# Kernel tuning notes

Measured on AMD Instinct MI355X. Metric: run time of the kernel, lower is better.

Reference implementation:

```python
import jax, jax.numpy as jnp
import numpy as np

N_NODES = 100000
N_EDGES = 3200000
D_IN, D_HID, D_OUT = 128, 128, 128


def setup_inputs() -> dict:
    key = jax.random.key(0)
    ks = jax.random.split(key, 8)
    x = jax.random.normal(ks[0], (N_NODES, D_IN), dtype=jnp.float32)
    edge_index = jax.random.randint(ks[1], (2, N_EDGES), 0, N_NODES, dtype=jnp.int64)
    def lin(k, din, dout):
        # glorot-ish init for GCNConv weight
        s = 1.0 / np.sqrt(din)
        return jax.random.uniform(k, (din, dout), jnp.float32, -s, s)
    W0 = lin(ks[2], D_IN, D_HID)
    b0 = jnp.zeros((D_HID,), jnp.float32)
    W1 = lin(ks[3], D_HID, D_HID)
    b1 = jnp.zeros((D_HID,), jnp.float32)
    W2 = lin(ks[4], D_HID, D_OUT)
    b2 = jnp.zeros((D_OUT,), jnp.float32)
    return {"x": x, "edge_index": edge_index, "W0": W0, "b0": b0,
            "W1": W1, "b1": b1, "W2": W2, "b2": b2}


def _gcn_norm(edge_index, n_nodes):
    # PyG gcn_norm with self-loops: deg over target index, sym normalization
    loop = jnp.arange(n_nodes, dtype=edge_index.dtype)
    src = jnp.concatenate([edge_index[0], loop])
    dst = jnp.concatenate([edge_index[1], loop])
    deg = jax.ops.segment_sum(jnp.ones_like(dst, dtype=jnp.float32), dst,
                              num_segments=n_nodes)
    dinv = jnp.where(deg > 0, jax.lax.rsqrt(deg), 0.0)
    norm = dinv[src] * dinv[dst]  # [E + N]
    return src, dst, norm


def _gcn_conv(h, src, dst, norm, W, b, n_nodes):
    h = h @ W                                   # [N, dout] transform first
    msg = h[src] * norm[:, None]                # gather + scale
    out = jax.ops.segment_sum(msg, dst, num_segments=n_nodes)  # scatter-add
    return out + b


def reference(x, edge_index, W0, b0, W1, b1, W2, b2):
    n = x.shape[0]
    src, dst, norm = _gcn_norm(edge_index, n)
    # layer 0
    h = jax.nn.relu(_gcn_conv(x, src, dst, norm, W0, b0, n))
    # residual middle layer (dropout is identity in eval mode)
    h = jax.nn.relu(_gcn_conv(h, src, dst, norm, W1, b1, n) + h)
    # output layer
    return _gcn_conv(h, src, dst, norm, W2, b2, n)
```

## Files before the change

### kernel.cpp

```cpp
#include <hip/hip_runtime.h>
#include <hip/hip_fp16.h>

#define D 128
typedef unsigned long long ull;
typedef _Float16 half8 __attribute__((ext_vector_type(8)));
typedef _Float16 half4v __attribute__((ext_vector_type(4)));
typedef float f32x4 __attribute__((ext_vector_type(4)));

#define KPOS(k4) (((k4) & ~31) + ((((k4) & 15) >> 2) << 3) + ((((k4) >> 4) & 1) << 2))

__global__ void k_zero_int(int* p, int n) {
  int i = blockIdx.x * blockDim.x + threadIdx.x;
  if (i < n) p[i] = 0;
}

__global__ void k_deg_count8(const int* __restrict__ ei, int* __restrict__ deg8,
                             int E, int N) {
  const int c = blockIdx.x & 7;
  const int m = blockIdx.x >> 3;
  const int nb = gridDim.x >> 3;
  const int cE = (E + 7) >> 3;
  const int base = c * cE;
  int lim = E - base;
  if (lim > cE) lim = cE;
  int* dg = deg8 + (size_t)c * N;
  for (int i = m * 256 + threadIdx.x; i < lim; i += nb * 256) {
    int d = __builtin_nontemporal_load(&ei[E + base + i]);
    atomicAdd(&dg[d], 1);
  }
}

__global__ void k_deg_reduce(const int* __restrict__ deg8, int* __restrict__ deg, int N) {
  int i = blockIdx.x * blockDim.x + threadIdx.x;
  if (i >= N) return;
  int s = 0;
#pragma unroll
  for (int c = 0; c < 8; c++) s += deg8[(size_t)c * N + i];
  deg[i] = s;
}

__global__ void k_scan_part(const int* __restrict__ deg, int* __restrict__ part, int n) {
  __shared__ int sd[256];
  int base = blockIdx.x * 2048 + threadIdx.x * 8;
  int s = 0;
#pragma unroll
  for (int k = 0; k < 8; k++) {
    int idx = base + k;
    if (idx < n) s += deg[idx];
  }
  sd[threadIdx.x] = s;
  __syncthreads();
  for (int off = 128; off > 0; off >>= 1) {
    if (threadIdx.x < off) sd[threadIdx.x] += sd[threadIdx.x + off];
    __syncthreads();
  }
  if (threadIdx.x == 0) part[blockIdx.x] = sd[0];
}

__global__ void k_scan_offsets(int* __restrict__ part, int nparts,
                               int* __restrict__ rowptr, int n) {
  __shared__ int sd[256];
  int v = (threadIdx.x < nparts) ? part[threadIdx.x] : 0;
  sd[threadIdx.x] = v;
  __syncthreads();
  for (int off = 1; off < 256; off <<= 1) {
    int t = (threadIdx.x >= off) ? sd[threadIdx.x - off] : 0;
    __syncthreads();
    sd[threadIdx.x] += t;
    __syncthreads();
  }
  if (threadIdx.x < nparts) part[threadIdx.x] = sd[threadIdx.x] - v;
  if (threadIdx.x == 0) rowptr[n] = sd[255];
}

__global__ void k_scan_final(const int* __restrict__ deg, const int* __restrict__ part,
                             int* __restrict__ rowptr, int n) {
  __shared__ int sd[256];
  int base = blockIdx.x * 2048 + threadIdx.x * 8;
  int loc[8];
  int s = 0;
#pragma unroll
  for (int k = 0; k < 8; k++) {
    int idx = base + k;
    loc[k] = (idx < n) ? deg[idx] : 0;
    s += loc[k];
  }
  sd[threadIdx.x] = s;
  __syncthreads();
  for (int off = 1; off < 256; off <<= 1) {
    int t = (threadIdx.x >= off) ? sd[threadIdx.x - off] : 0;
    __syncthreads();
    sd[threadIdx.x] += t;
    __syncthreads();
  }
  int run = part[blockIdx.x] + sd[threadIdx.x] - s;
#pragma unroll
  for (int k = 0; k < 8; k++) {
    int idx = base + k;
    if (idx < n) {
      rowptr[idx] = run;
      run += loc[k];
    }
  }
}

__global__ void k_dinv(const int* __restrict__ rowptr, float* __restrict__ dinv, int n) {
  int i = blockIdx.x * blockDim.x + threadIdx.x;
  if (i < n) dinv[i] = rsqrtf((float)(rowptr[i + 1] - rowptr[i]) + 1.0f);
}

__global__ void k_cursor8_init(const int* __restrict__ rowptr, const int* __restrict__ deg8,
                               int* __restrict__ cursor8, int N) {
  int v = blockIdx.x * blockDim.x + threadIdx.x;
  if (v >= N) return;
  int run = rowptr[v];
#pragma unroll
  for (int c = 0; c < 8; c++) {
    cursor8[(size_t)c * N + v] = run;
    run += deg8[(size_t)c * N + v];
  }
}

__global__ void k_csr_fill_1p(const int* __restrict__ ei, int* __restrict__ cursor8,
                              int* __restrict__ csr, int E, int N) {
  const int c = blockIdx.x & 7;
  const int m = blockIdx.x >> 3;
  const int nb = gridDim.x >> 3;
  const int cE = (E + 7) >> 3;
  const int base = c * cE;
  int lim = E - base;
  if (lim > cE) lim = cE;
  int* cur = cursor8 + (size_t)c * N;
  for (int i = m * 256 + threadIdx.x; i < lim; i += nb * 256) {
    int d = __builtin_nontemporal_load(&ei[E + base + i]);
    int s = __builtin_nontemporal_load(&ei[base + i]);
    int pos = atomicAdd(&cur[d], 1);
    csr[pos] = s;
  }
}

template <int HALF_IN>
__launch_bounds__(256, 2)
__global__ void k_gemm_mfma(const void* __restrict__ Av, const float* __restrict__ W,
                            const float* __restrict__ dinv, __half* __restrict__ Th, int n) {
  __shared__ _Float16 Al[128 * 136];
  __shared__ _Float16 Bl[128 * 136];
  const int tid = threadIdx.x;
  const int row0 = blockIdx.x * 128;

  if (HALF_IN) {
    const _Float16* A = (const _Float16*)Av;
    for (int i = tid; i < 2048; i += 256) {
      int r = i >> 4;
      int k8 = (i & 15) << 3;
      half8 v = {0, 0, 0, 0, 0, 0, 0, 0};
      if (row0 + r < n) v = *(const half8*)&A[(size_t)(row0 + r) * D + k8];
      *(half4v*)&Al[r * 136 + KPOS(k8)]     = (half4v){v[0], v[1], v[2], v[3]};
      *(half4v*)&Al[r * 136 + KPOS(k8 + 4)] = (half4v){v[4], v[5], v[6], v[7]};
    }
  } else {
    const float* A = (const float*)Av;
    for (int i = tid; i < 4096; i += 256) {
      int r = i >> 5;
      int k4 = (i & 31) << 2;
      float4 v = make_float4(0.f, 0.f, 0.f, 0.f);
      if (row0 + r < n) v = ((const float4*)A)[(size_t)(row0 + r) * 32 + (i & 31)];
      *(half4v*)&Al[r * 136 + KPOS(k4)] =
          (half4v){(_Float16)v.x, (_Float16)v.y, (_Float16)v.z, (_Float16)v.w};
    }
  }
  for (int i = tid; i < 4096; i += 256) {
    int c = i & 127;
    int k4 = (i >> 7) << 2;
    float w0 = W[(k4 + 0) * D + c];
    float w1 = W[(k4 + 1) * D + c];
    float w2 = W[(k4 + 2) * D + c];
    float w3 = W[(k4 + 3) * D + c];
    *(half4v*)&Bl[c * 136 + KPOS(k4)] =
        (half4v){(_Float16)w0, (_Float16)w1, (_Float16)w2, (_Float16)w3};
  }
  __syncthreads();

  const int w = tid >> 6;
  const int lane = tid & 63;
  const int g = lane >> 4;
  const int q = lane & 15;

  f32x4 acc[2][8];
#pragma unroll
  for (int mt = 0; mt < 2; mt++)
#pragma unroll
    for (int nt = 0; nt < 8; nt++) acc[mt][nt] = (f32x4){0.f, 0.f, 0.f, 0.f};

#pragma unroll
  for (int kt = 0; kt < 4; kt++) {
    half8 a[2], b[8];
#pragma unroll
    for (int mt = 0; mt < 2; mt++)
      a[mt] = *(const half8*)&Al[(w * 32 + mt * 16 + q) * 136 + kt * 32 + g * 8];
#pragma unroll
    for (int nt = 0; nt < 8; nt++)
      b[nt] = *(const half8*)&Bl[(nt * 16 + q) * 136 + kt * 32 + g * 8];
#pragma unroll
    for (int mt = 0; mt < 2; mt++)
#pragma unroll
      for (int nt = 0; nt < 8; nt++)
        acc[mt][nt] = __builtin_amdgcn_mfma_f32_16x16x32_f16(a[mt], b[nt], acc[mt][nt], 0, 0, 0);
  }

#pragma unroll
  for (int mt = 0; mt < 2; mt++) {
    int baseRow = row0 + w * 32 + mt * 16 + g * 4;
    float dv[4];
#pragma unroll
    for (int r = 0; r < 4; r++) dv[r] = (baseRow + r < n) ? dinv[baseRow + r] : 0.f;
#pragma unroll
    for (int nt = 0; nt < 8; nt++) {
      int col = nt * 16 + q;
#pragma unroll
      for (int r = 0; r < 4; r++) {
        int gr = baseRow + r;
        if (gr < n) Th[(size_t)gr * D + col] = (__half)(acc[mt][nt][r] * dv[r]);
      }
    }
  }
}

template <int MODE>
__launch_bounds__(256)
__global__ void k_aggregate(const int* __restrict__ rowptr, const int* __restrict__ csr,
                            const float* __restrict__ dinv, const __half* __restrict__ th,
                            const float* __restrict__ b, const __half* __restrict__ resh,
                            __half* __restrict__ outh, float* __restrict__ outf, int n) {
  int node = blockIdx.x * 16 + (threadIdx.x >> 4);
  if (node >= n) return;
  const int l16 = threadIdx.x & 15;

  int beg = rowptr[node];
  int end = rowptr[node + 1];
  float dd = dinv[node];

  const float4* t4 = (const float4*)th;

  float a0, a1, a2, a3, a4, a5, a6, a7;
  {
    float4 raw = t4[(size_t)node * 16 + l16];
    const __half2* hp = (const __half2*)&raw;
    float2 f0 = __half22float2(hp[0]);
    float2 f1 = __half22float2(hp[1]);
    float2 f2 = __half22float2(hp[2]);
    float2 f3 = __half22float2(hp[3]);
    a0 = f0.x; a1 = f0.y; a2 = f1.x; a3 = f1.y;
    a4 = f2.x; a5 = f2.y; a6 = f3.x; a7 = f3.y;
  }

#define ACC_ROW(raw)                                  \
  {                                                   \
    const __half2* hp = (const __half2*)&(raw);       \
    float2 f0 = __half22float2(hp[0]);                \
    float2 f1 = __half22float2(hp[1]);                \
    float2 f2 = __half22float2(hp[2]);                \
    float2 f3 = __half22float2(hp[3]);                \
    a0 += f0.x; a1 += f0.y; a2 += f1.x; a3 += f1.y;   \
    a4 += f2.x; a5 += f2.y; a6 += f3.x; a7 += f3.y;   \
  }

  int j = beg;
  for (; j + 8 <= end; j += 8) {
    float4 r0, r1, r2, r3, r4, r5, r6, r7;
    {
      int s0 = __builtin_nontemporal_load(&csr[j + 0]);
      int s1 = __builtin_nontemporal_load(&csr[j + 1]);
      int s2 = __builtin_nontemporal_load(&csr[j + 2]);
      int s3 = __builtin_nontemporal_load(&csr[j + 3]);
      int s4 = __builtin_nontemporal_load(&csr[j + 4]);
      int s5 = __builtin_nontemporal_load(&csr[j + 5]);
      int s6 = __builtin_nontemporal_load(&csr[j + 6]);
      int s7 = __builtin_nontemporal_load(&csr[j + 7]);
      r0 = t4[(size_t)(unsigned)s0 * 16 + l16];
      r1 = t4[(size_t)(unsigned)s1 * 16 + l16];
      r2 = t4[(size_t)(unsigned)s2 * 16 + l16];
      r3 = t4[(size_t)(unsigned)s3 * 16 + l16];
      r4 = t4[(size_t)(unsigned)s4 * 16 + l16];
      r5 = t4[(size_t)(unsigned)s5 * 16 + l16];
      r6 = t4[(size_t)(unsigned)s6 * 16 + l16];
      r7 = t4[(size_t)(unsigned)s7 * 16 + l16];
    }
    ACC_ROW(r0) ACC_ROW(r1) ACC_ROW(r2) ACC_ROW(r3)
    ACC_ROW(r4) ACC_ROW(r5) ACC_ROW(r6) ACC_ROW(r7)
  }
  for (; j + 4 <= end; j += 4) {
    int s0 = __builtin_nontemporal_load(&csr[j + 0]);
    int s1 = __builtin_nontemporal_load(&csr[j + 1]);
    int s2 = __builtin_nontemporal_load(&csr[j + 2]);
    int s3 = __builtin_nontemporal_load(&csr[j + 3]);
    float4 r0 = t4[(size_t)(unsigned)s0 * 16 + l16];
    float4 r1 = t4[(size_t)(unsigned)s1 * 16 + l16];
    float4 r2 = t4[(size_t)(unsigned)s2 * 16 + l16];
    float4 r3 = t4[(size_t)(unsigned)s3 * 16 + l16];
    ACC_ROW(r0) ACC_ROW(r1) ACC_ROW(r2) ACC_ROW(r3)
  }
  for (; j < end; ++j) {
    int s = __builtin_nontemporal_load(&csr[j]);
    float4 r = t4[(size_t)(unsigned)s * 16 + l16];
    ACC_ROW(r)
  }
#undef ACC_ROW

  const float4* b4 = (const float4*)b;
  float4 bb0 = b4[l16 * 2];
  float4 bb1 = b4[l16 * 2 + 1];
  float o0 = fmaf(a0, dd, bb0.x), o1 = fmaf(a1, dd, bb0.y);
  float o2 = fmaf(a2, dd, bb0.z), o3 = fmaf(a3, dd, bb0.w);
  float o4 = fmaf(a4, dd, bb1.x), o5 = fmaf(a5, dd, bb1.y);
  float o6 = fmaf(a6, dd, bb1.z), o7 = fmaf(a7, dd, bb1.w);

  if (MODE == 1) {
    float4 raw = ((const float4*)resh)[(size_t)node * 16 + l16];
    const __half2* hp = (const __half2*)&raw;
    float2 f0 = __half22float2(hp[0]);
    float2 f1 = __half22float2(hp[1]);
    float2 f2 = __half22float2(hp[2]);
    float2 f3 = __half22float2(hp[3]);
    o0 += f0.x; o1 += f0.y; o2 += f1.x; o3 += f1.y;
    o4 += f2.x; o5 += f2.y; o6 += f3.x; o7 += f3.y;
  }
  if (MODE == 0 || MODE == 1) {
    o0 = fmaxf(o0, 0.f); o1 = fmaxf(o1, 0.f); o2 = fmaxf(o2, 0.f); o3 = fmaxf(o3, 0.f);
    o4 = fmaxf(o4, 0.f); o5 = fmaxf(o5, 0.f); o6 = fmaxf(o6, 0.f); o7 = fmaxf(o7, 0.f);
    union { __half2 h[4]; float4 f; } pk;
    pk.h[0] = __floats2half2_rn(o0, o1);
    pk.h[1] = __floats2half2_rn(o2, o3);
    pk.h[2] = __floats2half2_rn(o4, o5);
    pk.h[3] = __floats2half2_rn(o6, o7);
    ((float4*)outh)[(size_t)node * 16 + l16] = pk.f;
  } else {
    ((float4*)outf)[(size_t)node * 32 + l16 * 2] = make_float4(o0, o1, o2, o3);
    ((float4*)outf)[(size_t)node * 32 + l16 * 2 + 1] = make_float4(o4, o5, o6, o7);
  }
}

extern "C" void kernel_launch(void* const* d_in, const int* in_sizes, int n_in,
                              void* d_out, int out_size, void* d_ws, size_t ws_size,
                              hipStream_t stream) {
  const float* x  = (const float*)d_in[0];
  const int*   ei = (const int*)d_in[1];
  const float* W0 = (const float*)d_in[2];
  const float* b0 = (const float*)d_in[3];
  const float* W1 = (const float*)d_in[4];
  const float* b1 = (const float*)d_in[5];
  const float* W2 = (const float*)d_in[6];
  const float* b2 = (const float*)d_in[7];
  float* out = (float*)d_out;

  const int N = in_sizes[0] / D;
  const int E = in_sizes[1] / 2;

  char* wsb = (char*)d_ws;
  auto alloc = [&](size_t bytes) {
    char* p = wsb;
    wsb += ((bytes + 255) & ~(size_t)255);
    return p;
  };
  int*    rowptr  = (int*)alloc((N + 1) * 4);
  int*    deg     = (int*)alloc(N * 4);
  int*    part    = (int*)alloc(256 * 4);
  float*  dinv    = (float*)alloc(N * 4);
  int*    deg8    = (int*)alloc((size_t)8 * N * 4);
  int*    cursor8 = (int*)alloc((size_t)8 * N * 4);
  int*    csr     = (int*)alloc((size_t)E * 4);
  __half* th      = (__half*)alloc((size_t)N * D * 2);
  __half* g1h     = (__half*)alloc((size_t)N * D * 2);
  __half* g2h     = (__half*)alloc((size_t)N * D * 2);

  dim3 b256(256);
  int gN   = (N + 255) / 256;
  int gN8  = (8 * N + 255) / 256;
  int gGem = (N + 127) / 128;
  int gAgg = (N + 15) / 16;
  int nparts = (N + 2047) / 2048;

  k_zero_int<<<gN8, b256, 0, stream>>>(deg8, 8 * N);
  k_deg_count8<<<8 * 256, b256, 0, stream>>>(ei, deg8, E, N);
  k_deg_reduce<<<gN, b256, 0, stream>>>(deg8, deg, N);
  k_scan_part<<<nparts, b256, 0, stream>>>(deg, part, N);
  k_scan_offsets<<<1, b256, 0, stream>>>(part, nparts, rowptr, N);
  k_scan_final<<<nparts, b256, 0, stream>>>(deg, part, rowptr, N);
  k_dinv<<<gN, b256, 0, stream>>>(rowptr, dinv, N);
  k_cursor8_init<<<gN, b256, 0, stream>>>(rowptr, deg8, cursor8, N);
  k_csr_fill_1p<<<8 * 256, b256, 0, stream>>>(ei, cursor8, csr, E, N);

  k_gemm_mfma<0><<<gGem, b256, 0, stream>>>(x, W0, dinv, th, N);
  k_aggregate<0><<<gAgg, b256, 0, stream>>>(rowptr, csr, dinv, th, b0, nullptr, g1h, nullptr, N);

  k_gemm_mfma<1><<<gGem, b256, 0, stream>>>(g1h, W1, dinv, th, N);
  k_aggregate<1><<<gAgg, b256, 0, stream>>>(rowptr, csr, dinv, th, b1, g1h, g2h, nullptr, N);

  k_gemm_mfma<1><<<gGem, b256, 0, stream>>>(g2h, W2, dinv, th, N);
  k_aggregate<2><<<gAgg, b256, 0, stream>>>(rowptr, csr, dinv, th, b2, nullptr, nullptr, out, N);
}
```

Measured before the change: 819.1 us.

## Fill CSR per-chunk contiguously then reorder into per-node rows

Instead of scattering source indices straight into the final per-node CSR rows, each of the 8 edge chunks now writes into its own chunk-major region, whose offsets come from a global scan over the 8*N per-chunk degrees. A follow-up reorder kernel then copies each node's eight segments into the final CSR. The aim is for the scatter writes to land in more local regions and so cut cache-line contention during the fill. In exchange it adds an extra E-sized buffer, a second scan, a copy kernel and a reorder pass in which one thread serially copies each node's edges.

```diff
diff --git a/kernel.cpp b/kernel.cpp
--- a/kernel.cpp
+++ b/kernel.cpp
@@ -12,6 +12,11 @@
 __global__ void k_zero_int(int* p, int n) {
   int i = blockIdx.x * blockDim.x + threadIdx.x;
   if (i < n) p[i] = 0;
+}
+
+__global__ void k_copy_int(const int* __restrict__ a, int* __restrict__ b, int n) {
+  int i = blockIdx.x * blockDim.x + threadIdx.x;
+  if (i < n) b[i] = a[i];
 }
 
 __global__ void k_deg_count8(const int* __restrict__ ei, int* __restrict__ deg8,
@@ -39,14 +44,15 @@
   deg[i] = s;
 }
 
-__global__ void k_scan_part(const int* __restrict__ deg, int* __restrict__ part, int n) {
+template <int ITEMS>
+__global__ void k_scan_part(const int* __restrict__ v, int* __restrict__ part, int n) {
   __shared__ int sd[256];
-  int base = blockIdx.x * 2048 + threadIdx.x * 8;
+  int base = blockIdx.x * (256 * ITEMS) + threadIdx.x * ITEMS;
   int s = 0;
 #pragma unroll
-  for (int k = 0; k < 8; k++) {
+  for (int k = 0; k < ITEMS; k++) {
     int idx = base + k;
-    if (idx < n) s += deg[idx];
+    if (idx < n) s += v[idx];
   }
   sd[threadIdx.x] = s;
   __syncthreads();
@@ -58,7 +64,7 @@
 }
 
 __global__ void k_scan_offsets(int* __restrict__ part, int nparts,
-                               int* __restrict__ rowptr, int n) {
+                               int* __restrict__ outp, int n) {
   __shared__ int sd[256];
   int v = (threadIdx.x < nparts) ? part[threadIdx.x] : 0;
   sd[threadIdx.x] = v;
@@ -70,19 +76,20 @@
     __syncthreads();
   }
   if (threadIdx.x < nparts) part[threadIdx.x] = sd[threadIdx.x] - v;
-  if (threadIdx.x == 0) rowptr[n] = sd[255];
-}
-
-__global__ void k_scan_final(const int* __restrict__ deg, const int* __restrict__ part,
-                             int* __restrict__ rowptr, int n) {
+  if (threadIdx.x == 0) outp[n] = sd[255];
+}
+
+template <int ITEMS>
+__global__ void k_scan_final(const int* __restrict__ v, const int* __restrict__ part,
+                             int* __restrict__ outp, int n) {
   __shared__ int sd[256];
-  int base = blockIdx.x * 2048 + threadIdx.x * 8;
-  int loc[8];
+  int base = blockIdx.x * (256 * ITEMS) + threadIdx.x * ITEMS;
+  int loc[ITEMS];
   int s = 0;
 #pragma unroll
-  for (int k = 0; k < 8; k++) {
+  for (int k = 0; k < ITEMS; k++) {
     int idx = base + k;
-    loc[k] = (idx < n) ? deg[idx] : 0;
+    loc[k] = (idx < n) ? v[idx] : 0;
     s += loc[k];
   }
   sd[threadIdx.x] = s;
@@ -95,34 +102,22 @@
   }
   int run = part[blockIdx.x] + sd[threadIdx.x] - s;
 #pragma unroll
-  for (int k = 0; k < 8; k++) {
+  for (int k = 0; k < ITEMS; k++) {
     int idx = base + k;
     if (idx < n) {
-      rowptr[idx] = run;
+      outp[idx] = run;
       run += loc[k];
     }
   }
 }
 
-__global__ void k_dinv(const int* __restrict__ rowptr, float* __restrict__ dinv, int n) {
+__global__ void k_dinv(const int* __restrict__ deg, float* __restrict__ dinv, int n) {
   int i = blockIdx.x * blockDim.x + threadIdx.x;
-  if (i < n) dinv[i] = rsqrtf((float)(rowptr[i + 1] - rowptr[i]) + 1.0f);
-}
-
-__global__ void k_cursor8_init(const int* __restrict__ rowptr, const int* __restrict__ deg8,
-                               int* __restrict__ cursor8, int N) {
-  int v = blockIdx.x * blockDim.x + threadIdx.x;
-  if (v >= N) return;
-  int run = rowptr[v];
-#pragma unroll
-  for (int c = 0; c < 8; c++) {
-    cursor8[(size_t)c * N + v] = run;
-    run += deg8[(size_t)c * N + v];
-  }
-}
-
-__global__ void k_csr_fill_1p(const int* __restrict__ ei, int* __restrict__ cursor8,
-                              int* __restrict__ csr, int E, int N) {
+  if (i < n) dinv[i] = rsqrtf((float)deg[i] + 1.0f);
+}
+
+__global__ void k_fill8(const int* __restrict__ ei, int* __restrict__ cursor8,
+                        int* __restrict__ csr8, int E, int N) {
   const int c = blockIdx.x & 7;
   const int m = blockIdx.x >> 3;
   const int nb = gridDim.x >> 3;
@@ -135,7 +130,20 @@
     int d = __builtin_nontemporal_load(&ei[E + base + i]);
     int s = __builtin_nontemporal_load(&ei[base + i]);
     int pos = atomicAdd(&cur[d], 1);
-    csr[pos] = s;
+    csr8[pos] = s;
+  }
+}
+
+__global__ void k_reorder(const int* __restrict__ S, const int* __restrict__ rowptr,
+                          const int* __restrict__ csr8, int* __restrict__ csr, int N) {
+  int v = blockIdx.x * blockDim.x + threadIdx.x;
+  if (v >= N) return;
+  int dst = rowptr[v];
+#pragma unroll
+  for (int c = 0; c < 8; c++) {
+    int b = S[(size_t)c * N + v];
+    int e = S[(size_t)c * N + v + 1];
+    for (int j = b; j < e; j++) csr[dst++] = __builtin_nontemporal_load(&csr8[j]);
   }
 }
 
@@ -365,30 +373,38 @@
   int*    rowptr  = (int*)alloc((N + 1) * 4);
   int*    deg     = (int*)alloc(N * 4);
   int*    part    = (int*)alloc(256 * 4);
+  int*    part2   = (int*)alloc(256 * 4);
   float*  dinv    = (float*)alloc(N * 4);
   int*    deg8    = (int*)alloc((size_t)8 * N * 4);
+  int*    S       = (int*)alloc(((size_t)8 * N + 1) * 4);
   int*    cursor8 = (int*)alloc((size_t)8 * N * 4);
+  int*    csr8    = (int*)alloc((size_t)E * 4);
   int*    csr     = (int*)alloc((size_t)E * 4);
   __half* th      = (__half*)alloc((size_t)N * D * 2);
   __half* g1h     = (__half*)alloc((size_t)N * D * 2);
   __half* g2h     = (__half*)alloc((size_t)N * D * 2);
 
   dim3 b256(256);
-  int gN   = (N + 255) / 256;
-  int gN8  = (8 * N + 255) / 256;
-  int gGem = (N + 127) / 128;
-  int gAgg = (N + 15) / 16;
-  int nparts = (N + 2047) / 2048;
+  int gN    = (N + 255) / 256;
+  int gN8   = (8 * N + 255) / 256;
+  int gGem  = (N + 127) / 128;
+  int gAgg  = (N + 15) / 16;
+  int np1   = (N + 2047) / 2048;
+  int np16  = (8 * N + 4095) / 4096;
 
   k_zero_int<<<gN8, b256, 0, stream>>>(deg8, 8 * N);
   k_deg_count8<<<8 * 256, b256, 0, stream>>>(ei, deg8, E, N);
   k_deg_reduce<<<gN, b256, 0, stream>>>(deg8, deg, N);
-  k_scan_part<<<nparts, b256, 0, stream>>>(deg, part, N);
-  k_scan_offsets<<<1, b256, 0, stream>>>(part, nparts, rowptr, N);
-  k_scan_final<<<nparts, b256, 0, stream>>>(deg, part, rowptr, N);
-  k_dinv<<<gN, b256, 0, stream>>>(rowptr, dinv, N);
-  k_cursor8_init<<<gN, b256, 0, stream>>>(rowptr, deg8, cursor8, N);
-  k_csr_fill_1p<<<8 * 256, b256, 0, stream>>>(ei, cursor8, csr, E, N);
+  k_scan_part<8><<<np1, b256, 0, stream>>>(deg, part, N);
+  k_scan_offsets<<<1, b256, 0, stream>>>(part, np1, rowptr, N);
+  k_scan_final<8><<<np1, b256, 0, stream>>>(deg, part, rowptr, N);
+  k_scan_part<16><<<np16, b256, 0, stream>>>(deg8, part2, 8 * N);
+  k_scan_offsets<<<1, b256, 0, stream>>>(part2, np16, S, 8 * N);
+  k_scan_final<16><<<np16, b256, 0, stream>>>(deg8, part2, S, 8 * N);
+  k_dinv<<<gN, b256, 0, stream>>>(deg, dinv, N);
+  k_copy_int<<<gN8, b256, 0, stream>>>(S, cursor8, 8 * N);
+  k_fill8<<<8 * 256, b256, 0, stream>>>(ei, cursor8, csr8, E, N);
+  k_reorder<<<gN, b256, 0, stream>>>(S, rowptr, csr8, csr, N);
 
   k_gemm_mfma<0><<<gGem, b256, 0, stream>>>(x, W0, dinv, th, N);
   k_aggregate<0><<<gAgg, b256, 0, stream>>>(rowptr, csr, dinv, th, b0, nullptr, g1h, nullptr, N);
```

New measurement: 834.6 us. No clear change (+1.9%).
